# Kernel tuning notes

Measured on AMD Instinct MI355X. Metric: run time of the kernel, lower is better.

Reference implementation:

```python
import math
import jax, jax.numpy as jnp
import numpy as np

D_MODEL = 1024
N_HEADS = 16
HEAD_DIM = D_MODEL // N_HEADS
ROPE_THETA = 10000.0


def setup_inputs() -> dict:
    key = jax.random.key(0)
    ks = jax.random.split(key, 5)
    B, T = 4, 2048
    # xavier-ish scale for weights
    w_scale = math.sqrt(2.0 / (D_MODEL + D_MODEL))
    return {
        "x": jax.random.normal(ks[0], (B, T, D_MODEL), dtype=jnp.float32),
        "Wq": jax.random.normal(ks[1], (D_MODEL, D_MODEL), dtype=jnp.float32) * w_scale,
        "Wk": jax.random.normal(ks[2], (D_MODEL, D_MODEL), dtype=jnp.float32) * w_scale,
        "Wv": jax.random.normal(ks[3], (D_MODEL, D_MODEL), dtype=jnp.float32) * w_scale,
        "Wo": jax.random.normal(ks[4], (D_MODEL, D_MODEL), dtype=jnp.float32) * w_scale,
    }


def _apply_rope(t, offset=0):
    # t: (B, H, T, Dh); standard half-rotation RoPE
    B, H, T, Dh = t.shape
    inv_freq = 1.0 / (ROPE_THETA ** (jnp.arange(0, Dh, 2, dtype=jnp.float32) / Dh))
    pos = jnp.arange(T, dtype=jnp.float32) + offset  # (T,)
    ang = pos[:, None] * inv_freq[None, :]           # (T, Dh/2)
    cos = jnp.concatenate([jnp.cos(ang), jnp.cos(ang)], axis=-1)  # (T, Dh)
    sin = jnp.concatenate([jnp.sin(ang), jnp.sin(ang)], axis=-1)
    t1, t2 = t[..., : Dh // 2], t[..., Dh // 2 :]
    rot = jnp.concatenate([-t2, t1], axis=-1)
    return t * cos + rot * sin


def _forward(x, Wq, Wk, Wv, Wo):
    B, T, _ = x.shape
    scale = 1.0 / math.sqrt(HEAD_DIM)

    def split_heads(y):  # (B,T,D) -> (B,H,T,Dh)
        return y.reshape(B, T, N_HEADS, HEAD_DIM).transpose(0, 2, 1, 3)

    q = split_heads(x @ Wq.T)
    k = split_heads(x @ Wk.T)
    v = split_heads(x @ Wv.T)

    q = _apply_rope(q)
    k = _apply_rope(k)

    # full materialized scores, as in the original manual SDPA
    scores = jnp.einsum("bhtd,bhsd->bhts", q, k) * scale  # (B,H,T,T)
    causal = jnp.triu(jnp.ones((T, T), dtype=bool), k=1)   # True = masked
    scores = jnp.where(causal[None, None], -jnp.inf, scores)
    attn = jax.nn.softmax(scores, axis=-1)
    attn = jnp.nan_to_num(attn, nan=0.0)
    out = jnp.einsum("bhts,bhsd->bhtd", attn, v)           # (B,H,T,Dh)
    out = out.transpose(0, 2, 1, 3).reshape(B, T, N_HEADS * HEAD_DIM)
    return out @ Wo.T


def reference(x, Wq, Wk, Wv, Wo):
    return _forward(x, Wq, Wk, Wv, Wo)
```

## Files before the change

### kernel.cpp

```cpp
#include <hip/hip_runtime.h>
#include <math.h>

typedef __bf16 bf16_t;
typedef __bf16 bf16x4 __attribute__((ext_vector_type(4)));
typedef __bf16 bf16x8 __attribute__((ext_vector_type(8)));
typedef float f32x4 __attribute__((ext_vector_type(4)));

#define MFMA16(a, b, c) __builtin_amdgcn_mfma_f32_16x16x32_bf16(a, b, c, 0, 0, 0)
#define GLD_LDS16(g, l)                                                                    \
    __builtin_amdgcn_global_load_lds((const __attribute__((address_space(1))) void*)(g),   \
                                     (__attribute__((address_space(3))) void*)(l), 16, 0, 0)

#define SM_SCALE_LOG2E 0.18033688011112042f
#define NEG_LOG2_10K_32 -0.41524101186092029f

__device__ __forceinline__ void fast_sincos(float ang, float* s, float* c) {
    float rev = ang * 0.15915494309189535f;
    rev = rev - floorf(rev);
    *s = __builtin_amdgcn_sinf(rev);
    *c = __builtin_amdgcn_cosf(rev);
}

__global__ void cvt_all(const float* __restrict__ x, const float* __restrict__ wq,
                        const float* __restrict__ wk, const float* __restrict__ wv,
                        const float* __restrict__ wo, bf16_t* __restrict__ out) {
    long i = ((long)blockIdx.x * 256 + threadIdx.x) * 4;
    const float* src;
    long off;
    const long M1 = 1048576;
    if (i < 8 * M1) { src = x;  off = i; }
    else if (i < 9 * M1)  { src = wq; off = i - 8 * M1; }
    else if (i < 10 * M1) { src = wk; off = i - 9 * M1; }
    else if (i < 11 * M1) { src = wv; off = i - 10 * M1; }
    else                  { src = wo; off = i - 11 * M1; }
    float4 v = *(const float4*)(src + off);
    out[i + 0] = (bf16_t)v.x;
    out[i + 1] = (bf16_t)v.y;
    out[i + 2] = (bf16_t)v.z;
    out[i + 3] = (bf16_t)v.w;
}

template <typename OutT>
__global__ __launch_bounds__(256) void gemm_bt(const bf16_t* __restrict__ A,
                                               const bf16_t* __restrict__ B,
                                               OutT* __restrict__ C,
                                               int M, int N, int K) {
    __shared__ __align__(16) bf16_t As[128 * 32];
    __shared__ __align__(16) bf16_t Bs[128 * 32];
    const int tid = threadIdx.x;
    const int lane = tid & 63, wave = tid >> 6;
    const int qd = lane >> 4, ln = lane & 15;
    const int m0 = blockIdx.y * 128, n0 = blockIdx.x * 128;
    const int wr = (wave >> 1) * 64, wc = (wave & 1) * 64;
    const int Kb = K * 2;

    f32x4 acc[4][4];
#pragma unroll
    for (int i = 0; i < 4; ++i)
#pragma unroll
        for (int j = 0; j < 4; ++j)
#pragma unroll
            for (int r = 0; r < 4; ++r) acc[i][j][r] = 0.f;

    const int off0 = wave * 2048 + lane * 16;
    const int off1 = off0 + 1024;
    const int r0 = off0 >> 6, c0 = off0 & 63;
    const int r1 = off1 >> 6, c1 = off1 & 63;

    for (int kt = 0; kt < K; kt += 32) {
        const char* Ab = (const char*)A + (size_t)m0 * Kb + kt * 2;
        const char* Bb = (const char*)B + (size_t)n0 * Kb + kt * 2;
        GLD_LDS16(Ab + (size_t)r0 * Kb + c0, (char*)As + wave * 2048);
        GLD_LDS16(Ab + (size_t)r1 * Kb + c1, (char*)As + wave * 2048 + 1024);
        GLD_LDS16(Bb + (size_t)r0 * Kb + c0, (char*)Bs + wave * 2048);
        GLD_LDS16(Bb + (size_t)r1 * Kb + c1, (char*)Bs + wave * 2048 + 1024);
        __syncthreads();
        bf16x8 af[4], bfr[4];
#pragma unroll
        for (int i = 0; i < 4; ++i)
            af[i] = *(const bf16x8*)(As + (wr + i * 16 + ln) * 32 + qd * 8);
#pragma unroll
        for (int j = 0; j < 4; ++j)
            bfr[j] = *(const bf16x8*)(Bs + (wc + j * 16 + ln) * 32 + qd * 8);
#pragma unroll
        for (int i = 0; i < 4; ++i)
#pragma unroll
            for (int j = 0; j < 4; ++j)
                acc[i][j] = MFMA16(af[i], bfr[j], acc[i][j]);
        __syncthreads();
    }
#pragma unroll
    for (int i = 0; i < 4; ++i)
#pragma unroll
        for (int j = 0; j < 4; ++j)
#pragma unroll
            for (int r = 0; r < 4; ++r) {
                int row = m0 + wr + i * 16 + qd * 4 + r;
                int col = n0 + wc + j * 16 + ln;
                C[(size_t)row * N + col] = (OutT)acc[i][j][r];
            }
}

__global__ __launch_bounds__(256) void gemm_qkv_rope(const bf16_t* __restrict__ A,
                                                     const bf16_t* __restrict__ B,
                                                     bf16_t* __restrict__ Qo,
                                                     bf16_t* __restrict__ Ko,
                                                     bf16_t* __restrict__ Vt,
                                                     int M, int K) {
    __shared__ __align__(16) bf16_t As[128 * 32];
    __shared__ __align__(16) bf16_t Bs[128 * 32];
    const int tid = threadIdx.x;
    const int lane = tid & 63, wave = tid >> 6;
    const int qd = lane >> 4, ln = lane & 15;
    const int m0 = blockIdx.y * 128, n0 = blockIdx.x * 128;
    const int wr = (wave >> 1) * 64, wc = (wave & 1) * 64;
    const int Kb = K * 2;

    f32x4 acc[4][4];
#pragma unroll
    for (int i = 0; i < 4; ++i)
#pragma unroll
        for (int j = 0; j < 4; ++j)
#pragma unroll
            for (int r = 0; r < 4; ++r) acc[i][j][r] = 0.f;

    const int off0 = wave * 2048 + lane * 16;
    const int off1 = off0 + 1024;
    const int r0 = off0 >> 6, c0 = off0 & 63;
    const int r1 = off1 >> 6, c1 = off1 & 63;

    for (int kt = 0; kt < K; kt += 32) {
        const char* Ab = (const char*)A + (size_t)m0 * Kb + kt * 2;
        const char* Bb = (const char*)B + (size_t)n0 * Kb + kt * 2;
        GLD_LDS16(Ab + (size_t)r0 * Kb + c0, (char*)As + wave * 2048);
        GLD_LDS16(Ab + (size_t)r1 * Kb + c1, (char*)As + wave * 2048 + 1024);
        GLD_LDS16(Bb + (size_t)r0 * Kb + c0, (char*)Bs + wave * 2048);
        GLD_LDS16(Bb + (size_t)r1 * Kb + c1, (char*)Bs + wave * 2048 + 1024);
        __syncthreads();
        bf16x8 af[4], bfr[4];
#pragma unroll
        for (int i = 0; i < 4; ++i)
            af[i] = *(const bf16x8*)(As + (wr + i * 16 + ln) * 32 + qd * 8);
#pragma unroll
        for (int j = 0; j < 4; ++j)
            bfr[j] = *(const bf16x8*)(Bs + (wc + j * 16 + ln) * 32 + qd * 8);
#pragma unroll
        for (int i = 0; i < 4; ++i)
#pragma unroll
            for (int j = 0; j < 4; ++j)
                acc[i][j] = MFMA16(af[i], bfr[j], acc[i][j]);
        __syncthreads();
    }

    if (n0 < 2048) {
        const bool isQ = (n0 < 1024);
        bf16_t* Out = isQ ? Qo : Ko;
        const float scale = isQ ? SM_SCALE_LOG2E : 1.0f;
        const int nc0 = n0 & 1023;
        const float inv0 = exp2f((float)ln * NEG_LOG2_10K_32);
        const float inv1 = exp2f((float)(ln + 16) * NEG_LOG2_10K_32);
#pragma unroll
        for (int i = 0; i < 4; ++i) {
#pragma unroll
            for (int r = 0; r < 4; ++r) {
                int row = m0 + wr + i * 16 + qd * 4 + r;
                int t = row & 2047, bb = row >> 11;
                float ft = (float)t;
                float s0, c0v, s1, c1v;
                fast_sincos(ft * inv0, &s0, &c0v);
                fast_sincos(ft * inv1, &s1, &c1v);
#pragma unroll
                for (int j = 0; j < 4; ++j) {
                    int col = nc0 + wc + j * 16 + ln;
                    int h = col >> 6, d = col & 63;
                    float sv = (j & 1) ? s1 : s0;
                    float cv = (j & 1) ? c1v : c0v;
                    float td = acc[i][j][r], tp = acc[i][j ^ 2][r];
                    float o = (j < 2) ? (td * cv - tp * sv) : (td * cv + tp * sv);
                    Out[((size_t)(bb * 16 + h) * 2048 + t) * 64 + d] = (bf16_t)(o * scale);
                }
            }
        }
    } else {
        const int nv0 = n0 - 2048;
#pragma unroll
        for (int i = 0; i < 4; ++i) {
            int tb = m0 + wr + i * 16 + qd * 4;
            int t = tb & 2047, bb = tb >> 11;
#pragma unroll
            for (int j = 0; j < 4; ++j) {
                int col = nv0 + wc + j * 16 + ln;
                int h = col >> 6, d = col & 63;
                bf16x4 pk;
#pragma unroll
                for (int r = 0; r < 4; ++r) pk[r] = (bf16_t)acc[i][j][r];
                *(bf16x4*)(Vt + ((size_t)(bb * 16 + h) * 64 + d) * 2048 + t) = pk;
            }
        }
    }
}

__global__ __launch_bounds__(256, 4) void attn_fwd(const bf16_t* __restrict__ Qg,
                                                   const bf16_t* __restrict__ Kg,
                                                   const bf16_t* __restrict__ Vtg,
                                                   bf16_t* __restrict__ Og) {
    __shared__ __align__(16) bf16_t Kt[64 * 72];
    __shared__ __align__(16) bf16_t Vl[64 * 72];
    __shared__ __align__(16) bf16_t Pl[4][16 * 72];
    const int id = blockIdx.x;
    const int bh = ((id & 7) << 3) | ((id >> 3) & 7);
    const int qt = 31 - (id >> 6);
    const int b = bh >> 4, h = bh & 15;
    const int tid = threadIdx.x, wave = tid >> 6, lane = tid & 63;
    const int qd = lane >> 4, ln = lane & 15;
    const int c0 = tid, c1 = 256 + tid;
    const int kr0r = c0 >> 3, kr0c = (c0 & 7) * 8;
    const int kr1r = c1 >> 3, kr1c = (c1 & 7) * 8;
    const bf16_t* Kbh = Kg + (size_t)bh * 2048 * 64;
    const bf16_t* Vbh = Vtg + (size_t)bh * 64 * 2048;

    bf16x8 vones;
#pragma unroll
    for (int i = 0; i < 8; ++i) vones[i] = (bf16_t)1.0f;

    const int q0 = qt * 64;
    const int wrow = q0 + wave * 16;
    const int njt = qt + 1;

    const bf16_t* Qbase = Qg + ((size_t)bh * 2048 + wrow + ln) * 64;
    bf16x8 aq0 = *(const bf16x8*)(Qbase + qd * 8);
    bf16x8 aq1 = *(const bf16x8*)(Qbase + 32 + qd * 8);

    f32x4 lsum = {0.f, 0.f, 0.f, 0.f};
    f32x4 o_acc[4];
#pragma unroll
    for (int c = 0; c < 4; ++c)
#pragma unroll
        for (int r = 0; r < 4; ++r) o_acc[c][r] = 0.f;

    int4 kr0, kr1, vr0, vr1;
    auto issue = [&](int j) {
        const bf16_t* kp = Kbh + (size_t)j * 64 * 64;
        const bf16_t* vp = Vbh + j * 64;
        kr0 = *(const int4*)(kp + kr0r * 64 + kr0c);
        kr1 = *(const int4*)(kp + kr1r * 64 + kr1c);
        vr0 = *(const int4*)(vp + (size_t)kr0r * 2048 + kr0c);
        vr1 = *(const int4*)(vp + (size_t)kr1r * 2048 + kr1c);
    };
    issue(0);

    for (int j = 0; j < njt; ++j) {
        __syncthreads();
        *(int4*)(Kt + kr0r * 72 + kr0c) = kr0;
        *(int4*)(Kt + kr1r * 72 + kr1c) = kr1;
        *(int4*)(Vl + kr0r * 72 + kr0c) = vr0;
        *(int4*)(Vl + kr1r * 72 + kr1c) = vr1;
        __syncthreads();
        if (j + 1 < njt) issue(j + 1);

        if (j * 64 > wrow + 15) continue;
        const int j64 = j * 64;

        f32x4 s[4];
#pragma unroll
        for (int st = 0; st < 4; ++st) {
            bf16x8 bk0 = *(const bf16x8*)(Kt + (st * 16 + ln) * 72 + qd * 8);
            bf16x8 bk1 = *(const bf16x8*)(Kt + (st * 16 + ln) * 72 + 32 + qd * 8);
            f32x4 t = {0.f, 0.f, 0.f, 0.f};
            t = MFMA16(aq0, bk0, t);
            t = MFMA16(aq1, bk1, t);
            s[st] = t;
        }

        if (j64 + 63 <= wrow) {
#pragma unroll
            for (int st = 0; st < 4; ++st)
#pragma unroll
                for (int r = 0; r < 4; ++r)
                    s[st][r] = __builtin_amdgcn_exp2f(s[st][r]);
        } else {
            int rowb = wrow + qd * 4;
#pragma unroll
            for (int st = 0; st < 4; ++st) {
                int col = j64 + st * 16 + ln;
#pragma unroll
                for (int r = 0; r < 4; ++r) {
                    float v = (col > rowb + r) ? -INFINITY : s[st][r];
                    s[st][r] = __builtin_amdgcn_exp2f(v);
                }
            }
        }

        bf16_t* P = &Pl[wave][0];
#pragma unroll
        for (int st = 0; st < 4; ++st)
#pragma unroll
            for (int r = 0; r < 4; ++r)
                P[(qd * 4 + r) * 72 + st * 16 + ln] = (bf16_t)s[st][r];

        bf16x8 ap0 = *(const bf16x8*)(P + ln * 72 + qd * 8);
        bf16x8 ap1 = *(const bf16x8*)(P + ln * 72 + 32 + qd * 8);
        lsum = MFMA16(ap0, vones, lsum);
        lsum = MFMA16(ap1, vones, lsum);
#pragma unroll
        for (int ct = 0; ct < 4; ++ct) {
            bf16x8 bv0 = *(const bf16x8*)(Vl + (ct * 16 + ln) * 72 + qd * 8);
            bf16x8 bv1 = *(const bf16x8*)(Vl + (ct * 16 + ln) * 72 + 32 + qd * 8);
            o_acc[ct] = MFMA16(ap0, bv0, o_acc[ct]);
            o_acc[ct] = MFMA16(ap1, bv1, o_acc[ct]);
        }
    }

    size_t obase = ((size_t)b * 2048 + wrow + qd * 4) * 1024 + h * 64;
    float rl[4];
#pragma unroll
    for (int r = 0; r < 4; ++r) rl[r] = __builtin_amdgcn_rcpf(lsum[r]);
#pragma unroll
    for (int ct = 0; ct < 4; ++ct)
#pragma unroll
        for (int r = 0; r < 4; ++r)
            Og[obase + (size_t)r * 1024 + ct * 16 + ln] = (bf16_t)(o_acc[ct][r] * rl[r]);
}

extern "C" void kernel_launch(void* const* d_in, const int* in_sizes, int n_in,
                              void* d_out, int out_size, void* d_ws, size_t ws_size,
                              hipStream_t stream) {
    (void)in_sizes; (void)n_in; (void)out_size; (void)ws_size;
    const float* x  = (const float*)d_in[0];
    const float* Wq = (const float*)d_in[1];
    const float* Wk = (const float*)d_in[2];
    const float* Wv = (const float*)d_in[3];
    const float* Wo = (const float*)d_in[4];
    char* ws = (char*)d_ws;
    const size_t MB = 1ull << 20;
    bf16_t* xb   = (bf16_t*)(ws + 0);
    bf16_t* wqb  = (bf16_t*)(ws + 16 * MB);
    bf16_t* wob  = (bf16_t*)(ws + 22 * MB);
    bf16_t* Qb   = (bf16_t*)(ws + 24 * MB);
    bf16_t* Kb   = (bf16_t*)(ws + 40 * MB);
    bf16_t* Vtb  = (bf16_t*)(ws + 56 * MB);
    bf16_t* AOb  = xb;

    cvt_all<<<dim3(12288), dim3(256), 0, stream>>>(x, Wq, Wk, Wv, Wo, (bf16_t*)ws);

    gemm_qkv_rope<<<dim3(24, 64), dim3(256), 0, stream>>>(xb, wqb, Qb, Kb, Vtb, 8192, 1024);

    attn_fwd<<<dim3(2048), dim3(256), 0, stream>>>(Qb, Kb, Vtb, AOb);

    gemm_bt<float><<<dim3(8, 64), dim3(256), 0, stream>>>(AOb, wob, (float*)d_out, 8192, 1024, 1024);
}
```

Baseline: 264.3 us.

## Use 128-row query tiles with paired causal tiles per attention block

The attention kernel now gives each wave 32 query rows (two 16-row fragments) instead of 16. Each K/V tile loaded into LDS therefore feeds twice as many MFMAs. Each block processes a pair of query tiles (qt and 15-qt), so the causal work per block is balanced, and the grid shrinks from 2048 to 512 blocks. The trade-off is higher register pressure, with the occupancy hint dropped from launch_bounds, and fewer blocks to spread across the CUs.

```diff
diff --git a/kernel.cpp b/kernel.cpp
--- a/kernel.cpp
+++ b/kernel.cpp
@@ -200,16 +200,16 @@
     }
 }
 
-__global__ __launch_bounds__(256, 4) void attn_fwd(const bf16_t* __restrict__ Qg,
-                                                   const bf16_t* __restrict__ Kg,
-                                                   const bf16_t* __restrict__ Vtg,
-                                                   bf16_t* __restrict__ Og) {
+__global__ __launch_bounds__(256) void attn_fwd(const bf16_t* __restrict__ Qg,
+                                                const bf16_t* __restrict__ Kg,
+                                                const bf16_t* __restrict__ Vtg,
+                                                bf16_t* __restrict__ Og) {
     __shared__ __align__(16) bf16_t Kt[64 * 72];
     __shared__ __align__(16) bf16_t Vl[64 * 72];
-    __shared__ __align__(16) bf16_t Pl[4][16 * 72];
+    __shared__ __align__(16) bf16_t Pl[4][32 * 72];
     const int id = blockIdx.x;
     const int bh = ((id & 7) << 3) | ((id >> 3) & 7);
-    const int qt = 31 - (id >> 6);
+    const int pair = (id >> 6) & 7;
     const int b = bh >> 4, h = bh & 15;
     const int tid = threadIdx.x, wave = tid >> 6, lane = tid & 63;
     const int qd = lane >> 4, ln = lane & 15;
@@ -223,103 +223,136 @@
 #pragma unroll
     for (int i = 0; i < 8; ++i) vones[i] = (bf16_t)1.0f;
 
-    const int q0 = qt * 64;
-    const int wrow = q0 + wave * 16;
-    const int njt = qt + 1;
-
-    const bf16_t* Qbase = Qg + ((size_t)bh * 2048 + wrow + ln) * 64;
-    bf16x8 aq0 = *(const bf16x8*)(Qbase + qd * 8);
-    bf16x8 aq1 = *(const bf16x8*)(Qbase + 32 + qd * 8);
-
-    f32x4 lsum = {0.f, 0.f, 0.f, 0.f};
-    f32x4 o_acc[4];
-#pragma unroll
-    for (int c = 0; c < 4; ++c)
-#pragma unroll
-        for (int r = 0; r < 4; ++r) o_acc[c][r] = 0.f;
-
-    int4 kr0, kr1, vr0, vr1;
-    auto issue = [&](int j) {
-        const bf16_t* kp = Kbh + (size_t)j * 64 * 64;
-        const bf16_t* vp = Vbh + j * 64;
-        kr0 = *(const int4*)(kp + kr0r * 64 + kr0c);
-        kr1 = *(const int4*)(kp + kr1r * 64 + kr1c);
-        vr0 = *(const int4*)(vp + (size_t)kr0r * 2048 + kr0c);
-        vr1 = *(const int4*)(vp + (size_t)kr1r * 2048 + kr1c);
-    };
-    issue(0);
-
-    for (int j = 0; j < njt; ++j) {
-        __syncthreads();
-        *(int4*)(Kt + kr0r * 72 + kr0c) = kr0;
-        *(int4*)(Kt + kr1r * 72 + kr1c) = kr1;
-        *(int4*)(Vl + kr0r * 72 + kr0c) = vr0;
-        *(int4*)(Vl + kr1r * 72 + kr1c) = vr1;
-        __syncthreads();
-        if (j + 1 < njt) issue(j + 1);
-
-        if (j * 64 > wrow + 15) continue;
-        const int j64 = j * 64;
-
-        f32x4 s[4];
-#pragma unroll
-        for (int st = 0; st < 4; ++st) {
-            bf16x8 bk0 = *(const bf16x8*)(Kt + (st * 16 + ln) * 72 + qd * 8);
-            bf16x8 bk1 = *(const bf16x8*)(Kt + (st * 16 + ln) * 72 + 32 + qd * 8);
-            f32x4 t = {0.f, 0.f, 0.f, 0.f};
-            t = MFMA16(aq0, bk0, t);
-            t = MFMA16(aq1, bk1, t);
-            s[st] = t;
-        }
-
-        if (j64 + 63 <= wrow) {
-#pragma unroll
-            for (int st = 0; st < 4; ++st)
+    for (int ph = 0; ph < 2; ++ph) {
+        const int qt = ph ? 15 - pair : pair;
+        const int q0 = qt * 128;
+        const int wrow = q0 + wave * 32;
+        const int njt = 2 * qt + 2;
+
+        bf16x8 aq[2][2];
+#pragma unroll
+        for (int f = 0; f < 2; ++f) {
+            const bf16_t* Qbase = Qg + ((size_t)bh * 2048 + wrow + f * 16 + ln) * 64;
+            aq[f][0] = *(const bf16x8*)(Qbase + qd * 8);
+            aq[f][1] = *(const bf16x8*)(Qbase + 32 + qd * 8);
+        }
+
+        f32x4 lsum[2];
+        f32x4 o_acc[2][4];
+#pragma unroll
+        for (int f = 0; f < 2; ++f) {
+#pragma unroll
+            for (int r = 0; r < 4; ++r) lsum[f][r] = 0.f;
+#pragma unroll
+            for (int c = 0; c < 4; ++c)
+#pragma unroll
+                for (int r = 0; r < 4; ++r) o_acc[f][c][r] = 0.f;
+        }
+
+        int4 kr0, kr1, vr0, vr1;
+        auto issue = [&](int j) {
+            const bf16_t* kp = Kbh + (size_t)j * 64 * 64;
+            const bf16_t* vp = Vbh + j * 64;
+            kr0 = *(const int4*)(kp + kr0r * 64 + kr0c);
+            kr1 = *(const int4*)(kp + kr1r * 64 + kr1c);
+            vr0 = *(const int4*)(vp + (size_t)kr0r * 2048 + kr0c);
+            vr1 = *(const int4*)(vp + (size_t)kr1r * 2048 + kr1c);
+        };
+        issue(0);
+
+        for (int j = 0; j < njt; ++j) {
+            __syncthreads();
+            *(int4*)(Kt + kr0r * 72 + kr0c) = kr0;
+            *(int4*)(Kt + kr1r * 72 + kr1c) = kr1;
+            *(int4*)(Vl + kr0r * 72 + kr0c) = vr0;
+            *(int4*)(Vl + kr1r * 72 + kr1c) = vr1;
+            __syncthreads();
+            if (j + 1 < njt) issue(j + 1);
+
+            if (j * 64 > wrow + 31) continue;
+            const int j64 = j * 64;
+
+            f32x4 s[2][4];
+#pragma unroll
+            for (int st = 0; st < 4; ++st) {
+                bf16x8 bk0 = *(const bf16x8*)(Kt + (st * 16 + ln) * 72 + qd * 8);
+                bf16x8 bk1 = *(const bf16x8*)(Kt + (st * 16 + ln) * 72 + 32 + qd * 8);
+#pragma unroll
+                for (int f = 0; f < 2; ++f) {
+                    f32x4 t = {0.f, 0.f, 0.f, 0.f};
+                    t = MFMA16(aq[f][0], bk0, t);
+                    t = MFMA16(aq[f][1], bk1, t);
+                    s[f][st] = t;
+                }
+            }
+
+            if (j64 + 63 <= wrow) {
+#pragma unroll
+                for (int f = 0; f < 2; ++f)
+#pragma unroll
+                    for (int st = 0; st < 4; ++st)
+#pragma unroll
+                        for (int r = 0; r < 4; ++r)
+                            s[f][st][r] = __builtin_amdgcn_exp2f(s[f][st][r]);
+            } else {
+#pragma unroll
+                for (int f = 0; f < 2; ++f) {
+                    int rowb = wrow + f * 16 + qd * 4;
+#pragma unroll
+                    for (int st = 0; st < 4; ++st) {
+                        int col = j64 + st * 16 + ln;
+#pragma unroll
+                        for (int r = 0; r < 4; ++r) {
+                            float v = (col > rowb + r) ? -INFINITY : s[f][st][r];
+                            s[f][st][r] = __builtin_amdgcn_exp2f(v);
+                        }
+                    }
+                }
+            }
+
+            bf16_t* P = &Pl[wave][0];
+#pragma unroll
+            for (int f = 0; f < 2; ++f)
+#pragma unroll
+                for (int st = 0; st < 4; ++st)
+#pragma unroll
+                    for (int r = 0; r < 4; ++r)
+                        P[(f * 16 + qd * 4 + r) * 72 + st * 16 + ln] = (bf16_t)s[f][st][r];
+
+            bf16x8 bv[4][2];
+#pragma unroll
+            for (int ct = 0; ct < 4; ++ct) {
+                bv[ct][0] = *(const bf16x8*)(Vl + (ct * 16 + ln) * 72 + qd * 8);
+                bv[ct][1] = *(const bf16x8*)(Vl + (ct * 16 + ln) * 72 + 32 + qd * 8);
+            }
+#pragma unroll
+            for (int f = 0; f < 2; ++f) {
+                bf16x8 ap0 = *(const bf16x8*)(P + (f * 16 + ln) * 72 + qd * 8);
+                bf16x8 ap1 = *(const bf16x8*)(P + (f * 16 + ln) * 72 + 32 + qd * 8);
+                lsum[f] = MFMA16(ap0, vones, lsum[f]);
+                lsum[f] = MFMA16(ap1, vones, lsum[f]);
+#pragma unroll
+                for (int ct = 0; ct < 4; ++ct) {
+                    o_acc[f][ct] = MFMA16(ap0, bv[ct][0], o_acc[f][ct]);
+                    o_acc[f][ct] = MFMA16(ap1, bv[ct][1], o_acc[f][ct]);
+                }
+            }
+        }
+
+#pragma unroll
+        for (int f = 0; f < 2; ++f) {
+            size_t obase = ((size_t)b * 2048 + wrow + f * 16 + qd * 4) * 1024 + h * 64;
+            float rl[4];
+#pragma unroll
+            for (int r = 0; r < 4; ++r) rl[r] = __builtin_amdgcn_rcpf(lsum[f][r]);
+#pragma unroll
+            for (int ct = 0; ct < 4; ++ct)
 #pragma unroll
                 for (int r = 0; r < 4; ++r)
-                    s[st][r] = __builtin_amdgcn_exp2f(s[st][r]);
-        } else {
-            int rowb = wrow + qd * 4;
-#pragma unroll
-            for (int st = 0; st < 4; ++st) {
-                int col = j64 + st * 16 + ln;
-#pragma unroll
-                for (int r = 0; r < 4; ++r) {
-                    float v = (col > rowb + r) ? -INFINITY : s[st][r];
-                    s[st][r] = __builtin_amdgcn_exp2f(v);
-                }
-            }
-        }
-
-        bf16_t* P = &Pl[wave][0];
-#pragma unroll
-        for (int st = 0; st < 4; ++st)
-#pragma unroll
-            for (int r = 0; r < 4; ++r)
-                P[(qd * 4 + r) * 72 + st * 16 + ln] = (bf16_t)s[st][r];
-
-        bf16x8 ap0 = *(const bf16x8*)(P + ln * 72 + qd * 8);
-        bf16x8 ap1 = *(const bf16x8*)(P + ln * 72 + 32 + qd * 8);
-        lsum = MFMA16(ap0, vones, lsum);
-        lsum = MFMA16(ap1, vones, lsum);
-#pragma unroll
-        for (int ct = 0; ct < 4; ++ct) {
-            bf16x8 bv0 = *(const bf16x8*)(Vl + (ct * 16 + ln) * 72 + qd * 8);
-            bf16x8 bv1 = *(const bf16x8*)(Vl + (ct * 16 + ln) * 72 + 32 + qd * 8);
-            o_acc[ct] = MFMA16(ap0, bv0, o_acc[ct]);
-            o_acc[ct] = MFMA16(ap1, bv1, o_acc[ct]);
+                    Og[obase + (size_t)r * 1024 + ct * 16 + ln] =
+                        (bf16_t)(o_acc[f][ct][r] * rl[r]);
         }
     }
-
-    size_t obase = ((size_t)b * 2048 + wrow + qd * 4) * 1024 + h * 64;
-    float rl[4];
-#pragma unroll
-    for (int r = 0; r < 4; ++r) rl[r] = __builtin_amdgcn_rcpf(lsum[r]);
-#pragma unroll
-    for (int ct = 0; ct < 4; ++ct)
-#pragma unroll
-        for (int r = 0; r < 4; ++r)
-            Og[obase + (size_t)r * 1024 + ct * 16 + ln] = (bf16_t)(o_acc[ct][r] * rl[r]);
 }
 
 extern "C" void kernel_launch(void* const* d_in, const int* in_sizes, int n_in,
@@ -345,7 +378,7 @@
 
     gemm_qkv_rope<<<dim3(24, 64), dim3(256), 0, stream>>>(xb, wqb, Qb, Kb, Vtb, 8192, 1024);
 
-    attn_fwd<<<dim3(2048), dim3(256), 0, stream>>>(Qb, Kb, Vtb, AOb);
+    attn_fwd<<<dim3(512), dim3(256), 0, stream>>>(Qb, Kb, Vtb, AOb);
 
     gemm_bt<float><<<dim3(8, 64), dim3(256), 0, stream>>>(AOb, wob, (float*)d_out, 8192, 1024, 1024);
 }
```

After: 257.4 us. 2.6% less time.
